# Performance work log

Hardware: AMD Instinct MI355X
Metric: run time of the kernel (lower is better)

## Reference

```python
import jax, jax.numpy as jnp
import numpy as np

S = 8192        # seq_length
H2 = 1024       # 2 * lstm_hidden_size
A = 2048        # attention_hidden_size
E = 768         # embedding_dim == pos_embedding_dim


def _bahdanau_weights(sentence, length, ctx, W_s, b_s, W_c, b_c, v, b_v):
    # sentence: [1, S, H2], ctx: [1, E_ctx]
    u = jnp.einsum('bsh,ha->bsa', sentence, W_s) + b_s \
        + (ctx @ W_c + b_c)[:, None, :]                    # [1, S, A]
    e = jnp.einsum('bsa,a->bs', jnp.tanh(u), v) + b_v       # [1, S]
    mask = jnp.arange(S)[None, :] >= length[:, None]        # [1, S] key mask
    e = jnp.where(mask, -jnp.inf, e)
    all_inf = jnp.all(mask, axis=1)                         # [1]
    # guard fully-masked rows so softmax stays finite, then zero them (matches torch)
    e_safe = jnp.where(all_inf[:, None], jnp.zeros_like(e), e)
    w = jax.nn.softmax(e_safe, axis=1)
    return jnp.where(all_inf[:, None], 0.0, w)              # [1, S]


def setup_inputs() -> dict:
    key = jax.random.key(0)
    ks = jax.random.split(key, 24)
    f = jax.random.normal
    sc_s = 1.0 / np.sqrt(H2)
    sc_c = 1.0 / np.sqrt(E)
    sc_v = 1.0 / np.sqrt(A)
    inp = {
        'sentence': f(ks[0], (1, S, H2), jnp.float32),
        'length': jax.random.randint(ks[1], (1,), 0, S),
        'pos_embedding': f(ks[2], (1, E), jnp.float32),
        'cardinal_phrase_embedding': f(ks[3], (1, E), jnp.float32),
        'headline_embedding': f(ks[4], (1, E), jnp.float32),
    }
    i = 5
    for tag in ('p', 'c', 'h'):
        inp[f'W_sent_{tag}'] = f(ks[i], (H2, A), jnp.float32) * sc_s; i += 1
        inp[f'b_sent_{tag}'] = f(ks[i], (A,), jnp.float32) * sc_s; i += 1
        inp[f'W_ctx_{tag}'] = f(ks[i], (E, A), jnp.float32) * sc_c; i += 1
        inp[f'b_ctx_{tag}'] = f(ks[i], (A,), jnp.float32) * sc_c; i += 1
        inp[f'v_{tag}'] = f(ks[i], (A,), jnp.float32) * sc_v; i += 1
        inp[f'bv_{tag}'] = f(ks[i], (), jnp.float32) * sc_v; i += 1
    return inp


def reference(sentence, length, pos_embedding, cardinal_phrase_embedding,
              headline_embedding,
              W_sent_p, b_sent_p, W_ctx_p, b_ctx_p, v_p, bv_p,
              W_sent_c, b_sent_c, W_ctx_c, b_ctx_c, v_c, bv_c,
              W_sent_h, b_sent_h, W_ctx_h, b_ctx_h, v_h, bv_h):
    w_pos = _bahdanau_weights(sentence, length, pos_embedding,
                              W_sent_p, b_sent_p, W_ctx_p, b_ctx_p, v_p, bv_p)
    w_card = _bahdanau_weights(sentence, length, cardinal_phrase_embedding,
                               W_sent_c, b_sent_c, W_ctx_c, b_ctx_c, v_c, bv_c)
    w_head = _bahdanau_weights(sentence, length, headline_embedding,
                               W_sent_h, b_sent_h, W_ctx_h, b_ctx_h, v_h, bv_h)
    fused = (w_pos + w_card + w_head) / 3.0                 # [1, S]
    return jnp.einsum('bs,bsh->bh', fused, sentence)        # [1, H2]
```

## Files before the change

### kernel.cpp

```cpp
#include <hip/hip_runtime.h>
#include <hip/hip_bf16.h>
#include <stdint.h>


namespace {

constexpr int S = 8192;
constexpr int H = 1024;
constexpr int A = 2048;
constexpr int E = 768;

typedef __bf16 bf16x8 __attribute__((ext_vector_type(8)));
typedef float f32x4 __attribute__((ext_vector_type(4)));

__device__ __forceinline__ void gl_lds16(const void* g, void* l) {
  __builtin_amdgcn_global_load_lds(
      (const __attribute__((address_space(1))) void*)g,
      (__attribute__((address_space(3))) void*)l, 16, 0, 0);
}

__global__ __launch_bounds__(256)
void k_prep(const float* __restrict__ sentence, __bf16* __restrict__ sentB,
            const float* __restrict__ Wp, const float* __restrict__ Wc_s,
            const float* __restrict__ Wh, __bf16* __restrict__ WtB,
            float* __restrict__ e_arr,
            const int* __restrict__ length, float* __restrict__ out, int n_out) {
  __shared__ float tile[64][65];
  int b = blockIdx.x;
  int t = threadIdx.x;

  if (b < 4096) {
    int len = min(max(length[0], 0), S);
    int lenp = (len + 63) & ~63;
    if (b * 2 >= lenp) return;
    int g = b * 256 + t;
    const float4* s4 = (const float4*)sentence + (size_t)g * 2;
    float4 a = s4[0], c = s4[1];
    bf16x8 o;
    o[0] = (__bf16)a.x; o[1] = (__bf16)a.y; o[2] = (__bf16)a.z; o[3] = (__bf16)a.w;
    o[4] = (__bf16)c.x; o[5] = (__bf16)c.y; o[6] = (__bf16)c.z; o[7] = (__bf16)c.w;
    *((bf16x8*)sentB + g) = o;
  } else if (b < 5632) {
    int r = b - 4096;
    int head = r >> 9; r &= 511;
    const float* W = head == 0 ? Wp : (head == 1 ? Wc_s : Wh);
    __bf16* dst = WtB + (size_t)head * A * H;
    int a0 = (r & 31) * 64;
    int k0 = (r >> 5) * 64;
#pragma unroll
    for (int i = 0; i < 16; ++i) {
      int idx = t + i * 256;
      int rr = idx >> 6, cc = idx & 63;
      tile[cc][rr] = W[(size_t)(k0 + rr) * A + a0 + cc];
    }
    __syncthreads();
#pragma unroll
    for (int i = 0; i < 16; ++i) {
      int idx = t + i * 256;
      int al = idx >> 6, kl = idx & 63;
      dst[(size_t)(a0 + al) * H + k0 + kl] = (__bf16)tile[al][kl];
    }
  } else {
    int idx = (b - 5632) * 256 + t;
    float4 z = {0.f, 0.f, 0.f, 0.f};
    int total = 6144 + (n_out >> 2);
    for (int i = idx; i < total; i += 2048) {
      if (i < 6144) ((float4*)e_arr)[i] = z;
      else ((float4*)out)[i - 6144] = z;
    }
  }
}

__global__ __launch_bounds__(256)
void k_gemm_e(const __bf16* __restrict__ sentB, const __bf16* __restrict__ WtB,
              const float* __restrict__ ctx_p, const float* __restrict__ ctx_c,
              const float* __restrict__ ctx_h,
              const float* __restrict__ Wcx_p, const float* __restrict__ Wcx_c,
              const float* __restrict__ Wcx_h,
              const float* __restrict__ bs_p, const float* __restrict__ bs_c,
              const float* __restrict__ bs_h,
              const float* __restrict__ bc_p, const float* __restrict__ bc_c,
              const float* __restrict__ bc_h,
              const float* __restrict__ v_p, const float* __restrict__ v_c,
              const float* __restrict__ v_h,
              const int* __restrict__ length, float* __restrict__ e_out) {
  int m0 = blockIdx.x * 64;
  int len = min(max(length[0], 0), S);
  if (m0 >= len) return;
  int n0 = blockIdx.y * 128;
  int head = blockIdx.z;
  const float* v  = head == 0 ? v_p : (head == 1 ? v_c : v_h);
  const __bf16* Wt = WtB + (size_t)head * A * H;
  float* e_h = e_out + head * S;

  __shared__ __align__(16) __bf16 lsA[4 * 2048];
  __shared__ __align__(16) __bf16 lsB[4 * 4096];
  __shared__ float cb_part[256];
  __shared__ float e_part[64];

  int tid = threadIdx.x;
  if (tid < 64) e_part[tid] = 0.f;

  int lane = tid & 63;
  int wave = tid >> 6;
  int wm = wave >> 1, wn = wave & 1;
  int quad = lane >> 4, l16 = lane & 15;

  f32x4 acc[2][4];
#pragma unroll
  for (int i = 0; i < 2; ++i)
#pragma unroll
    for (int j = 0; j < 4; ++j) acc[i][j] = (f32x4){0.f, 0.f, 0.f, 0.f};

  const __bf16* gA0 = sentB + (size_t)(m0 + (tid >> 2)) * H + ((tid & 3) * 8);
  const __bf16* gB0 = Wt + (size_t)(n0 + (tid >> 2)) * H + ((tid & 3) * 8);
  const __bf16* gB1 = gB0 + (size_t)64 * H;

#define STAGE(bufi, kk)                                           \
  do {                                                            \
    gl_lds16(gA0 + (kk), lsA + (bufi) * 2048 + tid * 8);          \
    gl_lds16(gB0 + (kk), lsB + (bufi) * 4096 + tid * 8);          \
    gl_lds16(gB1 + (kk), lsB + (bufi) * 4096 + 2048 + tid * 8);   \
  } while (0)

#define COMPUTE(bufi)                                                                          \
  do {                                                                                         \
    bf16x8 af[2], bfv[4];                                                                      \
    _Pragma("unroll")                                                                          \
    for (int i = 0; i < 2; ++i)                                                                \
      af[i] = *(const bf16x8*)&lsA[(bufi) * 2048 + (wm * 32 + i * 16 + l16) * 32 + quad * 8];  \
    _Pragma("unroll")                                                                          \
    for (int j = 0; j < 4; ++j)                                                                \
      bfv[j] = *(const bf16x8*)&lsB[(bufi) * 4096 + (wn * 64 + j * 16 + l16) * 32 + quad * 8]; \
    _Pragma("unroll")                                                                          \
    for (int i = 0; i < 2; ++i)                                                                \
      _Pragma("unroll")                                                                        \
      for (int j = 0; j < 4; ++j)                                                              \
        acc[i][j] = __builtin_amdgcn_mfma_f32_16x16x32_bf16(af[i], bfv[j], acc[i][j], 0, 0, 0);\
  } while (0)

  STAGE(0, 0);
  STAGE(1, 32);
  STAGE(2, 64);
  {
    const float* ctx = head == 0 ? ctx_p : (head == 1 ? ctx_c : ctx_h);
    const float* Wc  = head == 0 ? Wcx_p : (head == 1 ? Wcx_c : Wcx_h);
    int col = n0 + (tid & 127);
    int e0 = (tid >> 7) * (E / 2);
    float s = 0.f;
#pragma unroll 8
    for (int e = e0; e < e0 + E / 2; ++e) s = fmaf(ctx[e], Wc[(size_t)e * A + col], s);
    cb_part[tid] = s;
  }

#pragma unroll 1
  for (int t = 0; t < 29; ++t) {
    asm volatile("s_waitcnt vmcnt(6)");
    __builtin_amdgcn_s_barrier();
    __builtin_amdgcn_sched_barrier(0);
    STAGE((t + 3) & 3, (t + 3) * 32);
    COMPUTE(t & 3);
  }
  asm volatile("s_waitcnt vmcnt(6)");
  __builtin_amdgcn_s_barrier();
  __builtin_amdgcn_sched_barrier(0);
  COMPUTE(1);
  asm volatile("s_waitcnt vmcnt(3)");
  __builtin_amdgcn_s_barrier();
  __builtin_amdgcn_sched_barrier(0);
  COMPUTE(2);
  asm volatile("s_waitcnt vmcnt(0)");
  __builtin_amdgcn_s_barrier();
  __builtin_amdgcn_sched_barrier(0);
  COMPUTE(3);

#undef STAGE
#undef COMPUTE

  const float* bs = head == 0 ? bs_p : (head == 1 ? bs_c : bs_h);
  const float* bc = head == 0 ? bc_p : (head == 1 ? bc_c : bc_h);
  float vj[4], cbj[4];
#pragma unroll
  for (int j = 0; j < 4; ++j) {
    int cl = wn * 64 + j * 16 + l16;
    int col = n0 + cl;
    vj[j] = v[col];
    cbj[j] = cb_part[cl] + cb_part[128 + cl] + bs[col] + bc[col];
  }
#pragma unroll
  for (int i = 0; i < 2; ++i) {
#pragma unroll
    for (int r = 0; r < 4; ++r) {
      float p = 0.f;
#pragma unroll
      for (int j = 0; j < 4; ++j) {
        float u = acc[i][j][r] + cbj[j];
        float ex = __expf(2.f * u);
        float th = 1.f - 2.f / (ex + 1.f);
        p = fmaf(th, vj[j], p);
      }
      p += __shfl_xor(p, 1);
      p += __shfl_xor(p, 2);
      p += __shfl_xor(p, 4);
      p += __shfl_xor(p, 8);
      if (l16 == 0) atomicAdd(&e_part[wm * 32 + i * 16 + quad * 4 + r], p);
    }
  }
  __syncthreads();
  if (tid < 64) atomicAdd(&e_h[m0 + tid], e_part[tid]);
}

__global__ void k_out(const float* __restrict__ sent, const float* __restrict__ e_arr,
                      const int* __restrict__ length, float* __restrict__ out) {
  int len = min(max(length[0], 0), S);
  int r0 = blockIdx.x * 16;
  if (r0 >= len) return;
  int tid = threadIdx.x;

  __shared__ float red[3][4];
  __shared__ float sstat[6];
  __shared__ float wrow[16];

#pragma unroll
  for (int h = 0; h < 3; ++h) {
    const float* e_h = e_arr + h * S;
    float m = -3.4e38f;
    for (int s = tid; s < len; s += 256) m = fmaxf(m, e_h[s]);
#pragma unroll
    for (int o = 32; o >= 1; o >>= 1) m = fmaxf(m, __shfl_xor(m, o));
    if ((tid & 63) == 0) red[h][tid >> 6] = m;
  }
  __syncthreads();
  if (tid < 3) sstat[tid * 2] = fmaxf(fmaxf(red[tid][0], red[tid][1]),
                                      fmaxf(red[tid][2], red[tid][3]));
  __syncthreads();
#pragma unroll
  for (int h = 0; h < 3; ++h) {
    const float* e_h = e_arr + h * S;
    float mm = sstat[h * 2];
    float ss = 0.f;
    for (int s = tid; s < len; s += 256) ss += __expf(e_h[s] - mm);
#pragma unroll
    for (int o = 32; o >= 1; o >>= 1) ss += __shfl_xor(ss, o);
    if ((tid & 63) == 0) red[h][tid >> 6] = ss;
  }
  __syncthreads();
  if (tid < 3) sstat[tid * 2 + 1] = red[tid][0] + red[tid][1] + red[tid][2] + red[tid][3];
  __syncthreads();

  if (tid < 16 && r0 + tid < len) {
    int r = r0 + tid;
    wrow[tid] = (__expf(e_arr[r] - sstat[0]) / sstat[1] +
                 __expf(e_arr[S + r] - sstat[2]) / sstat[3] +
                 __expf(e_arr[2 * S + r] - sstat[4]) / sstat[5]) * (1.f / 3.f);
  }
  __syncthreads();

  int col = tid * 4;
  int rend = min(r0 + 16, len);
  float4 acc = {0.f, 0.f, 0.f, 0.f};
  for (int r = r0; r < rend; ++r) {
    float w = wrow[r - r0];
    float4 x = *(const float4*)(sent + (size_t)r * H + col);
    acc.x = fmaf(w, x.x, acc.x);
    acc.y = fmaf(w, x.y, acc.y);
    acc.z = fmaf(w, x.z, acc.z);
    acc.w = fmaf(w, x.w, acc.w);
  }
  atomicAdd(&out[col + 0], acc.x);
  atomicAdd(&out[col + 1], acc.y);
  atomicAdd(&out[col + 2], acc.z);
  atomicAdd(&out[col + 3], acc.w);
}

}

extern "C" void kernel_launch(void* const* d_in, const int* in_sizes, int n_in,
                              void* d_out, int out_size, void* d_ws, size_t ws_size,
                              hipStream_t stream) {
  const float* sentence = (const float*)d_in[0];
  const int* length     = (const int*)d_in[1];
  const float* ctx_p = (const float*)d_in[2];
  const float* ctx_c = (const float*)d_in[3];
  const float* ctx_h = (const float*)d_in[4];
  const float* W_s[3] = {(const float*)d_in[5],  (const float*)d_in[11], (const float*)d_in[17]};
  const float* b_s[3] = {(const float*)d_in[6],  (const float*)d_in[12], (const float*)d_in[18]};
  const float* W_c[3] = {(const float*)d_in[7],  (const float*)d_in[13], (const float*)d_in[19]};
  const float* b_c[3] = {(const float*)d_in[8],  (const float*)d_in[14], (const float*)d_in[20]};
  const float* v_[3]  = {(const float*)d_in[9],  (const float*)d_in[15], (const float*)d_in[21]};
  float* out = (float*)d_out;

  char* ws = (char*)d_ws;
  __bf16* sentB = (__bf16*)(ws);
  __bf16* WtB   = (__bf16*)(ws + 16777216);
  float* e_arr  = (float*)(ws + 29384704);

  k_prep<<<5640, 256, 0, stream>>>(sentence, sentB,
                                   W_s[0], W_s[1], W_s[2], WtB,
                                   e_arr, length, out, out_size);
  k_gemm_e<<<dim3(S / 64, A / 128, 3), 256, 0, stream>>>(
      sentB, WtB,
      ctx_p, ctx_c, ctx_h,
      W_c[0], W_c[1], W_c[2],
      b_s[0], b_s[1], b_s[2],
      b_c[0], b_c[1], b_c[2],
      v_[0], v_[1], v_[2], length, e_arr);
  k_out<<<S / 16, 256, 0, stream>>>(sentence, e_arr, length, out);
}
```

Baseline: 251.5 us.

## Precompute context bias in prep kernel and shrink GEMM N tile to 64

```diff
diff --git a/kernel.cpp b/kernel.cpp
--- a/kernel.cpp
+++ b/kernel.cpp
@@ -23,7 +23,15 @@
 void k_prep(const float* __restrict__ sentence, __bf16* __restrict__ sentB,
             const float* __restrict__ Wp, const float* __restrict__ Wc_s,
             const float* __restrict__ Wh, __bf16* __restrict__ WtB,
-            float* __restrict__ e_arr,
+            const float* __restrict__ ctx_p, const float* __restrict__ ctx_c,
+            const float* __restrict__ ctx_h,
+            const float* __restrict__ Wcx_p, const float* __restrict__ Wcx_c,
+            const float* __restrict__ Wcx_h,
+            const float* __restrict__ bs_p, const float* __restrict__ bs_c,
+            const float* __restrict__ bs_h,
+            const float* __restrict__ bc_p, const float* __restrict__ bc_c,
+            const float* __restrict__ bc_h,
+            float* __restrict__ ctxb_q, float* __restrict__ e_arr,
             const int* __restrict__ length, float* __restrict__ out, int n_out) {
   __shared__ float tile[64][65];
   int b = blockIdx.x;
@@ -60,8 +68,27 @@
       int al = idx >> 6, kl = idx & 63;
       dst[(size_t)(a0 + al) * H + k0 + kl] = (__bf16)tile[al][kl];
     }
+  } else if (b < 5728) {
+    int r = b - 5632;
+    int head = r >> 5;
+    int sub = r & 31;
+    int ablk = sub & 7;
+    int eq = sub >> 3;
+    const float* ctx = head == 0 ? ctx_p : (head == 1 ? ctx_c : ctx_h);
+    const float* Wc  = head == 0 ? Wcx_p : (head == 1 ? Wcx_c : Wcx_h);
+    int a = ablk * 256 + t;
+    float s = 0.f;
+    if (eq == 0) {
+      const float* bs = head == 0 ? bs_p : (head == 1 ? bs_c : bs_h);
+      const float* bc = head == 0 ? bc_p : (head == 1 ? bc_c : bc_h);
+      s = bs[a] + bc[a];
+    }
+    int e0 = eq * 192;
+#pragma unroll 8
+    for (int e = e0; e < e0 + 192; ++e) s = fmaf(ctx[e], Wc[(size_t)e * A + a], s);
+    ctxb_q[eq * 3 * A + head * A + a] = s;
   } else {
-    int idx = (b - 5632) * 256 + t;
+    int idx = (b - 5728) * 256 + t;
     float4 z = {0.f, 0.f, 0.f, 0.f};
     int total = 6144 + (n_out >> 2);
     for (int i = idx; i < total; i += 2048) {
@@ -73,29 +100,21 @@
 
 __global__ __launch_bounds__(256)
 void k_gemm_e(const __bf16* __restrict__ sentB, const __bf16* __restrict__ WtB,
-              const float* __restrict__ ctx_p, const float* __restrict__ ctx_c,
-              const float* __restrict__ ctx_h,
-              const float* __restrict__ Wcx_p, const float* __restrict__ Wcx_c,
-              const float* __restrict__ Wcx_h,
-              const float* __restrict__ bs_p, const float* __restrict__ bs_c,
-              const float* __restrict__ bs_h,
-              const float* __restrict__ bc_p, const float* __restrict__ bc_c,
-              const float* __restrict__ bc_h,
+              const float* __restrict__ ctxb_q,
               const float* __restrict__ v_p, const float* __restrict__ v_c,
               const float* __restrict__ v_h,
               const int* __restrict__ length, float* __restrict__ e_out) {
   int m0 = blockIdx.x * 64;
   int len = min(max(length[0], 0), S);
   if (m0 >= len) return;
-  int n0 = blockIdx.y * 128;
+  int n0 = blockIdx.y * 64;
   int head = blockIdx.z;
   const float* v  = head == 0 ? v_p : (head == 1 ? v_c : v_h);
   const __bf16* Wt = WtB + (size_t)head * A * H;
   float* e_h = e_out + head * S;
 
   __shared__ __align__(16) __bf16 lsA[4 * 2048];
-  __shared__ __align__(16) __bf16 lsB[4 * 4096];
-  __shared__ float cb_part[256];
+  __shared__ __align__(16) __bf16 lsB[4 * 2048];
   __shared__ float e_part[64];
 
   int tid = threadIdx.x;
@@ -106,66 +125,53 @@
   int wm = wave >> 1, wn = wave & 1;
   int quad = lane >> 4, l16 = lane & 15;
 
-  f32x4 acc[2][4];
+  f32x4 acc[2][2];
 #pragma unroll
   for (int i = 0; i < 2; ++i)
 #pragma unroll
-    for (int j = 0; j < 4; ++j) acc[i][j] = (f32x4){0.f, 0.f, 0.f, 0.f};
+    for (int j = 0; j < 2; ++j) acc[i][j] = (f32x4){0.f, 0.f, 0.f, 0.f};
 
   const __bf16* gA0 = sentB + (size_t)(m0 + (tid >> 2)) * H + ((tid & 3) * 8);
   const __bf16* gB0 = Wt + (size_t)(n0 + (tid >> 2)) * H + ((tid & 3) * 8);
-  const __bf16* gB1 = gB0 + (size_t)64 * H;
 
 #define STAGE(bufi, kk)                                           \
   do {                                                            \
     gl_lds16(gA0 + (kk), lsA + (bufi) * 2048 + tid * 8);          \
-    gl_lds16(gB0 + (kk), lsB + (bufi) * 4096 + tid * 8);          \
-    gl_lds16(gB1 + (kk), lsB + (bufi) * 4096 + 2048 + tid * 8);   \
+    gl_lds16(gB0 + (kk), lsB + (bufi) * 2048 + tid * 8);          \
   } while (0)
 
 #define COMPUTE(bufi)                                                                          \
   do {                                                                                         \
-    bf16x8 af[2], bfv[4];                                                                      \
+    bf16x8 af[2], bfv[2];                                                                      \
     _Pragma("unroll")                                                                          \
     for (int i = 0; i < 2; ++i)                                                                \
       af[i] = *(const bf16x8*)&lsA[(bufi) * 2048 + (wm * 32 + i * 16 + l16) * 32 + quad * 8];  \
     _Pragma("unroll")                                                                          \
-    for (int j = 0; j < 4; ++j)                                                                \
-      bfv[j] = *(const bf16x8*)&lsB[(bufi) * 4096 + (wn * 64 + j * 16 + l16) * 32 + quad * 8]; \
+    for (int j = 0; j < 2; ++j)                                                                \
+      bfv[j] = *(const bf16x8*)&lsB[(bufi) * 2048 + (wn * 32 + j * 16 + l16) * 32 + quad * 8]; \
     _Pragma("unroll")                                                                          \
     for (int i = 0; i < 2; ++i)                                                                \
       _Pragma("unroll")                                                                        \
-      for (int j = 0; j < 4; ++j)                                                              \
+      for (int j = 0; j < 2; ++j)                                                              \
         acc[i][j] = __builtin_amdgcn_mfma_f32_16x16x32_bf16(af[i], bfv[j], acc[i][j], 0, 0, 0);\
   } while (0)
 
   STAGE(0, 0);
   STAGE(1, 32);
   STAGE(2, 64);
-  {
-    const float* ctx = head == 0 ? ctx_p : (head == 1 ? ctx_c : ctx_h);
-    const float* Wc  = head == 0 ? Wcx_p : (head == 1 ? Wcx_c : Wcx_h);
-    int col = n0 + (tid & 127);
-    int e0 = (tid >> 7) * (E / 2);
-    float s = 0.f;
-#pragma unroll 8
-    for (int e = e0; e < e0 + E / 2; ++e) s = fmaf(ctx[e], Wc[(size_t)e * A + col], s);
-    cb_part[tid] = s;
-  }
-
 #pragma unroll 1
   for (int t = 0; t < 29; ++t) {
-    asm volatile("s_waitcnt vmcnt(6)");
+    asm volatile("s_waitcnt vmcnt(4)");
     __builtin_amdgcn_s_barrier();
     __builtin_amdgcn_sched_barrier(0);
     STAGE((t + 3) & 3, (t + 3) * 32);
     COMPUTE(t & 3);
   }
-  asm volatile("s_waitcnt vmcnt(6)");
+  asm volatile("s_waitcnt vmcnt(4)");
   __builtin_amdgcn_s_barrier();
   __builtin_amdgcn_sched_barrier(0);
   COMPUTE(1);
-  asm volatile("s_waitcnt vmcnt(3)");
+  asm volatile("s_waitcnt vmcnt(2)");
   __builtin_amdgcn_s_barrier();
   __builtin_amdgcn_sched_barrier(0);
   COMPUTE(2);
@@ -177,15 +183,13 @@
 #undef STAGE
 #undef COMPUTE
 
-  const float* bs = head == 0 ? bs_p : (head == 1 ? bs_c : bs_h);
-  const float* bc = head == 0 ? bc_p : (head == 1 ? bc_c : bc_h);
-  float vj[4], cbj[4];
-#pragma unroll
-  for (int j = 0; j < 4; ++j) {
-    int cl = wn * 64 + j * 16 + l16;
-    int col = n0 + cl;
+  float vj[2], cbj[2];
+#pragma unroll
+  for (int j = 0; j < 2; ++j) {
+    int col = n0 + wn * 32 + j * 16 + l16;
     vj[j] = v[col];
-    cbj[j] = cb_part[cl] + cb_part[128 + cl] + bs[col] + bc[col];
+    cbj[j] = ctxb_q[head * A + col] + ctxb_q[3 * A + head * A + col] +
+             ctxb_q[6 * A + head * A + col] + ctxb_q[9 * A + head * A + col];
   }
 #pragma unroll
   for (int i = 0; i < 2; ++i) {
@@ -193,7 +197,7 @@
     for (int r = 0; r < 4; ++r) {
       float p = 0.f;
 #pragma unroll
-      for (int j = 0; j < 4; ++j) {
+      for (int j = 0; j < 2; ++j) {
         float u = acc[i][j][r] + cbj[j];
         float ex = __expf(2.f * u);
         float th = 1.f - 2.f / (ex + 1.f);
@@ -291,19 +295,19 @@
   float* out = (float*)d_out;
 
   char* ws = (char*)d_ws;
-  __bf16* sentB = (__bf16*)(ws);
-  __bf16* WtB   = (__bf16*)(ws + 16777216);
-  float* e_arr  = (float*)(ws + 29384704);
-
-  k_prep<<<5640, 256, 0, stream>>>(sentence, sentB,
+  __bf16* sentB  = (__bf16*)(ws);
+  __bf16* WtB    = (__bf16*)(ws + 16777216);
+  float* ctxb_q  = (float*)(ws + 29360128);
+  float* e_arr   = (float*)(ws + 29458432);
+
+  k_prep<<<5736, 256, 0, stream>>>(sentence, sentB,
                                    W_s[0], W_s[1], W_s[2], WtB,
-                                   e_arr, length, out, out_size);
-  k_gemm_e<<<dim3(S / 64, A / 128, 3), 256, 0, stream>>>(
-      sentB, WtB,
-      ctx_p, ctx_c, ctx_h,
-      W_c[0], W_c[1], W_c[2],
-      b_s[0], b_s[1], b_s[2],
-      b_c[0], b_c[1], b_c[2],
-      v_[0], v_[1], v_[2], length, e_arr);
+                                   ctx_p, ctx_c, ctx_h,
+                                   W_c[0], W_c[1], W_c[2],
+                                   b_s[0], b_s[1], b_s[2],
+                                   b_c[0], b_c[1], b_c[2], ctxb_q, e_arr,
+                                   length, out, out_size);
+  k_gemm_e<<<dim3(S / 64, A / 64, 3), 256, 0, stream>>>(sentB, WtB, ctxb_q,
+                                                        v_[0], v_[1], v_[2], length, e_arr);
   k_out<<<S / 16, 256, 0, stream>>>(sentence, e_arr, length, out);
 }
```

New measurement: 230.3 us. 1.09x faster.
